# Kernel tuning notes

Measured on AMD Instinct MI355X. Metric: run time of the kernel, lower is better.

## Reference

```python
import jax, jax.numpy as jnp
import numpy as np

B, V, FIN, COUT, K = 16, 20000, 64, 64, 16


def setup_inputs() -> dict:
    key = jax.random.key(0)
    k1, k2, k3, k4 = jax.random.split(key, 4)
    x = jax.random.normal(k1, (B, V, FIN), dtype=jnp.float32)
    Wx = jax.random.normal(k2, (FIN, COUT), dtype=jnp.float32) * (1.0 / np.sqrt(FIN))
    Wn = jax.random.normal(k3, (FIN, COUT), dtype=jnp.float32) * (1.0 / np.sqrt(FIN))
    b = jnp.zeros((COUT,), dtype=jnp.float32)
    # neighbor indices into the padded input: 0 is the zero-padding row, 1..V are real vertices
    neighbor = jax.random.randint(k4, (V, K), 0, V + 1, dtype=jnp.int32)
    return {"x": x, "Wx": Wx, "Wn": Wn, "b": b, "neighbor": neighbor}


def reference(x, Wx, Wn, b, neighbor):
    # x: [B, V, Fin]; neighbor: [V, K] indices into padded (V+1) vertex axis
    Bsz, Vn, Fin = x.shape
    pad = jnp.zeros((Bsz, 1, Fin), dtype=x.dtype)
    padded = jnp.concatenate([pad, x], axis=1)            # [B, V+1, Fin]
    nb = padded[:, neighbor, :]                            # [B, V, K, Fin] (gather)
    nb_mean = jnp.mean(nb, axis=2)                         # sum/K == mean (zeros included)
    out = jnp.einsum('bvf,fc->bvc', x, Wx) \
        + jnp.einsum('bvf,fc->bvc', nb_mean, Wn) + b
    return out
```

## Files before the change

kernel.cpp:

```cpp
#include <hip/hip_runtime.h>
#include <hip/hip_bf16.h>

#define BATCH 16
#define NV    20000
#define FIN   64
#define NCOUT 64
#define NK    16
#define TOTROWS  (BATCH * NV)
#define NTILES   (TOTROWS / 16)

typedef __attribute__((ext_vector_type(8))) short bf16x8;
typedef __attribute__((ext_vector_type(4))) float f32x4;
typedef __attribute__((ext_vector_type(4))) unsigned short u16x4;

__device__ __forceinline__ short f2b(float f) {
    __hip_bfloat16 h = __float2bfloat16(f);
    return __builtin_bit_cast(short, h);
}

__global__ __launch_bounds__(256, 3) void convnet_gemm(
    const float* __restrict__ x,
    const float* __restrict__ Wx,
    const float* __restrict__ Wn,
    const float* __restrict__ bias,
    __hip_bfloat16* __restrict__ z,
    float* __restrict__ out)
{
    const int lane = threadIdx.x & 63;
    const int m    = lane & 15;
    const int quad = lane >> 4;

    bf16x8 bf[8][2];
#pragma unroll
    for (int t = 0; t < 8; ++t) {
        const float* W = (t < 4) ? Wx : Wn;
        const float scale = (t < 4) ? 1.0f : (1.0f / 16.0f);
        const int c = 4 * m + (t & 3);
#pragma unroll
        for (int h = 0; h < 2; ++h) {
            bf16x8 fr;
#pragma unroll
            for (int j = 0; j < 8; ++j) {
                const int f = 32 * h + quad * 8 + j;
                fr[j] = f2b(W[f * NCOUT + c] * scale);
            }
            bf[t][h] = fr;
        }
    }
    float bias_q[4];
#pragma unroll
    for (int t = 0; t < 4; ++t) bias_q[t] = bias[4 * m + t];

    const int nwaves = (gridDim.x * blockDim.x) >> 6;
    const int gw = (blockIdx.x * blockDim.x + threadIdx.x) >> 6;

    int rt = __builtin_amdgcn_readfirstlane(gw);
    const float* xt0 = x + (size_t)rt * (16 * FIN) + (size_t)m * FIN + quad * 8;
    float4 La0 = ((const float4*)xt0)[0];
    float4 La1 = ((const float4*)xt0)[1];
    float4 Lb0 = ((const float4*)(xt0 + 32))[0];
    float4 Lb1 = ((const float4*)(xt0 + 32))[1];

    for (;;) {
        bf16x8 af0, af1;
        af0[0] = f2b(La0.x); af0[1] = f2b(La0.y); af0[2] = f2b(La0.z); af0[3] = f2b(La0.w);
        af0[4] = f2b(La1.x); af0[5] = f2b(La1.y); af0[6] = f2b(La1.z); af0[7] = f2b(La1.w);
        af1[0] = f2b(Lb0.x); af1[1] = f2b(Lb0.y); af1[2] = f2b(Lb0.z); af1[3] = f2b(Lb0.w);
        af1[4] = f2b(Lb1.x); af1[5] = f2b(Lb1.y); af1[6] = f2b(Lb1.z); af1[7] = f2b(Lb1.w);

        const int rtn = rt + nwaves;
        const bool more = rtn < NTILES;
        float4 Na0, Na1, Nb0, Nb1;
        if (more) {
            const float* xn = x + (size_t)rtn * (16 * FIN) + (size_t)m * FIN + quad * 8;
            Na0 = ((const float4*)xn)[0];
            Na1 = ((const float4*)xn)[1];
            Nb0 = ((const float4*)(xn + 32))[0];
            Nb1 = ((const float4*)(xn + 32))[1];
        }

        f32x4 acc[8];
#pragma unroll
        for (int t = 0; t < 8; ++t) acc[t] = (f32x4){0.f, 0.f, 0.f, 0.f};
#pragma unroll
        for (int t = 0; t < 8; ++t)
            acc[t] = __builtin_amdgcn_mfma_f32_16x16x32_bf16(af0, bf[t][0], acc[t], 0, 0, 0);
#pragma unroll
        for (int t = 0; t < 8; ++t)
            acc[t] = __builtin_amdgcn_mfma_f32_16x16x32_bf16(af1, bf[t][1], acc[t], 0, 0, 0);

        const size_t rbase = (size_t)rt * 16 + quad * 4;
#pragma unroll
        for (int r = 0; r < 4; ++r) {
            const size_t orow = (rbase + r) * NCOUT + 4 * m;
            float4 o;
            o.x = acc[0][r] + bias_q[0];
            o.y = acc[1][r] + bias_q[1];
            o.z = acc[2][r] + bias_q[2];
            o.w = acc[3][r] + bias_q[3];
            *(float4*)(out + orow) = o;
            u16x4 zz;
            zz.x = (unsigned short)f2b(acc[4][r]);
            zz.y = (unsigned short)f2b(acc[5][r]);
            zz.z = (unsigned short)f2b(acc[6][r]);
            zz.w = (unsigned short)f2b(acc[7][r]);
            *(u16x4*)(z + orow) = zz;
        }

        if (!more) break;
        rt = __builtin_amdgcn_readfirstlane(rtn);
        La0 = Na0; La1 = Na1; Lb0 = Nb0; Lb1 = Nb1;
    }
}

__global__ __launch_bounds__(256, 6) void convnet_gather(
    const int* __restrict__ nbr,
    const __hip_bfloat16* __restrict__ z,
    float* __restrict__ out)
{
    const int lane = threadIdx.x & 63;
    const int s    = lane >> 4;
    const int c    = lane & 15;
    const int xcd  = blockIdx.x & 7;
    const int bi   = blockIdx.x >> 3;
    const int wl   = bi * (256 >> 6) + (threadIdx.x >> 6);
    const int WPX  = (gridDim.x >> 3) * (256 >> 6);

    const int nvoff = s * (NK * 4);
    const int zcol  = c * 8;
    const int GROUPS = (2 * NV) / 4;

    for (int g = wl; g < GROUPS; g += WPX) {
        const int gu = __builtin_amdgcn_readfirstlane(g);
        const int bl = (gu >= NV / 4) ? 1 : 0;
        const int b  = 2 * xcd + bl;
        const int v0 = gu * 4 - bl * NV;
        const int row0 = b * NV + v0;

        const int* nb = (const int*)((const char*)nbr + (size_t)v0 * (NK * 4) + nvoff);
        int id[NK];
#pragma unroll
        for (int k = 0; k < NK; ++k) id[k] = nb[k];

        const char* zb = (const char*)z + (size_t)b * NV * 128;
        float a0 = 0.f, a1 = 0.f, a2 = 0.f, a3 = 0.f;
#pragma unroll
        for (int k = 0; k < NK; ++k) {
            const int idx = id[k];
            int sel = idx - 1;
            sel = sel < 0 ? 0 : sel;
            const uint2 d = *(const uint2*)(zb + (size_t)(unsigned)(sel * 128 + zcol));
            const unsigned dx = idx ? d.x : 0u;
            const unsigned dy = idx ? d.y : 0u;
            a0 += __builtin_bit_cast(float, dx << 16);
            a1 += __builtin_bit_cast(float, dx & 0xFFFF0000u);
            a2 += __builtin_bit_cast(float, dy << 16);
            a3 += __builtin_bit_cast(float, dy & 0xFFFF0000u);
        }

        float4* o = (float4*)(out + (size_t)(row0 + s) * NCOUT + 4 * c);
        float4 ov = *o;
        ov.x += a0; ov.y += a1; ov.z += a2; ov.w += a3;
        *o = ov;
    }
}

extern "C" void kernel_launch(void* const* d_in, const int* in_sizes, int n_in,
                              void* d_out, int out_size, void* d_ws, size_t ws_size,
                              hipStream_t stream) {
    const float* x    = (const float*)d_in[0];
    const float* Wx   = (const float*)d_in[1];
    const float* Wn   = (const float*)d_in[2];
    const float* bias = (const float*)d_in[3];
    const int*   nbr  = (const int*)d_in[4];
    float* out = (float*)d_out;

    __hip_bfloat16* z = (__hip_bfloat16*)d_ws;

    hipLaunchKernelGGL(convnet_gemm, dim3(768), dim3(256), 0, stream,
                       x, Wx, Wn, bias, z, out);
    hipLaunchKernelGGL(convnet_gather, dim3(1536), dim3(256), 0, stream,
                       nbr, z, out);
}
```

Baseline: 225.1 us.

## Split GEMM accumulators, drop prefetch, XCD-map tiles, vectorize neighbor index loads

The GEMM kernel now maps tiles to XCDs in contiguous chunks and removes the software prefetch of the next tile. It computes the output half and the z half in two separate 4-accumulator phases to lower register pressure, with occupancy and grid raised to match. The gather kernel loads each row's 16 neighbor indices as four int4 loads instead of per-lane scalar loads, and issues the output read before the gather loop. Grid sizes and launch bounds are increased. Dropping the prefetch may expose global load latency, which the higher occupancy is meant to hide.

```diff
diff --git a/kernel.cpp b/kernel.cpp
--- a/kernel.cpp
+++ b/kernel.cpp
@@ -8,6 +8,7 @@
 #define NK    16
 #define TOTROWS  (BATCH * NV)
 #define NTILES   (TOTROWS / 16)
+#define TPX      (NTILES / 8)
 
 typedef __attribute__((ext_vector_type(8))) short bf16x8;
 typedef __attribute__((ext_vector_type(4))) float f32x4;
@@ -18,7 +19,7 @@
     return __builtin_bit_cast(short, h);
 }
 
-__global__ __launch_bounds__(256, 3) void convnet_gemm(
+__global__ __launch_bounds__(256, 4) void convnet_gemm(
     const float* __restrict__ x,
     const float* __restrict__ Wx,
     const float* __restrict__ Wn,
@@ -51,69 +52,75 @@
 #pragma unroll
     for (int t = 0; t < 4; ++t) bias_q[t] = bias[4 * m + t];
 
-    const int nwaves = (gridDim.x * blockDim.x) >> 6;
-    const int gw = (blockIdx.x * blockDim.x + threadIdx.x) >> 6;
+    const int xcd = blockIdx.x & 7;
+    const int bi  = blockIdx.x >> 3;
+    const int wl  = bi * 4 + ((int)threadIdx.x >> 6);
+    const int WPX = (gridDim.x >> 3) * 4;
 
-    int rt = __builtin_amdgcn_readfirstlane(gw);
-    const float* xt0 = x + (size_t)rt * (16 * FIN) + (size_t)m * FIN + quad * 8;
-    float4 La0 = ((const float4*)xt0)[0];
-    float4 La1 = ((const float4*)xt0)[1];
-    float4 Lb0 = ((const float4*)(xt0 + 32))[0];
-    float4 Lb1 = ((const float4*)(xt0 + 32))[1];
+    for (int t0 = wl; t0 < TPX; t0 += WPX) {
+        const int rt = __builtin_amdgcn_readfirstlane(xcd * TPX + t0);
+        const float* xt =
+            x + (size_t)rt * (16 * FIN) + (size_t)m * FIN + quad * 8;
 
-    for (;;) {
+        const float4 La0 = ((const float4*)xt)[0];
+        const float4 La1 = ((const float4*)xt)[1];
+        const float4 Lb0 = ((const float4*)(xt + 32))[0];
+        const float4 Lb1 = ((const float4*)(xt + 32))[1];
+
         bf16x8 af0, af1;
         af0[0] = f2b(La0.x); af0[1] = f2b(La0.y); af0[2] = f2b(La0.z); af0[3] = f2b(La0.w);
         af0[4] = f2b(La1.x); af0[5] = f2b(La1.y); af0[6] = f2b(La1.z); af0[7] = f2b(La1.w);
         af1[0] = f2b(Lb0.x); af1[1] = f2b(Lb0.y); af1[2] = f2b(Lb0.z); af1[3] = f2b(Lb0.w);
         af1[4] = f2b(Lb1.x); af1[5] = f2b(Lb1.y); af1[6] = f2b(Lb1.z); af1[7] = f2b(Lb1.w);
 
-        const int rtn = rt + nwaves;
-        const bool more = rtn < NTILES;
-        float4 Na0, Na1, Nb0, Nb1;
-        if (more) {
-            const float* xn = x + (size_t)rtn * (16 * FIN) + (size_t)m * FIN + quad * 8;
-            Na0 = ((const float4*)xn)[0];
-            Na1 = ((const float4*)xn)[1];
-            Nb0 = ((const float4*)(xn + 32))[0];
-            Nb1 = ((const float4*)(xn + 32))[1];
+        const size_t rbase = (size_t)rt * 16 + quad * 4;
+
+        {
+            f32x4 accP[4];
+#pragma unroll
+            for (int t = 0; t < 4; ++t) accP[t] = (f32x4){0.f, 0.f, 0.f, 0.f};
+#pragma unroll
+            for (int t = 0; t < 4; ++t)
+                accP[t] = __builtin_amdgcn_mfma_f32_16x16x32_bf16(af0, bf[t][0], accP[t], 0, 0, 0);
+#pragma unroll
+            for (int t = 0; t < 4; ++t)
+                accP[t] = __builtin_amdgcn_mfma_f32_16x16x32_bf16(af1, bf[t][1], accP[t], 0, 0, 0);
+#pragma unroll
+            for (int r = 0; r < 4; ++r) {
+                const size_t orow = (rbase + r) * NCOUT + 4 * m;
+                float4 o;
+                o.x = accP[0][r] + bias_q[0];
+                o.y = accP[1][r] + bias_q[1];
+                o.z = accP[2][r] + bias_q[2];
+                o.w = accP[3][r] + bias_q[3];
+                *(float4*)(out + orow) = o;
+            }
         }
-
-        f32x4 acc[8];
+        {
+            f32x4 accZ[4];
 #pragma unroll
-        for (int t = 0; t < 8; ++t) acc[t] = (f32x4){0.f, 0.f, 0.f, 0.f};
+            for (int t = 0; t < 4; ++t) accZ[t] = (f32x4){0.f, 0.f, 0.f, 0.f};
 #pragma unroll
-        for (int t = 0; t < 8; ++t)
-            acc[t] = __builtin_amdgcn_mfma_f32_16x16x32_bf16(af0, bf[t][0], acc[t], 0, 0, 0);
+            for (int t = 0; t < 4; ++t)
+                accZ[t] = __builtin_amdgcn_mfma_f32_16x16x32_bf16(af0, bf[t + 4][0], accZ[t], 0, 0, 0);
 #pragma unroll
-        for (int t = 0; t < 8; ++t)
-            acc[t] = __builtin_amdgcn_mfma_f32_16x16x32_bf16(af1, bf[t][1], acc[t], 0, 0, 0);
-
-        const size_t rbase = (size_t)rt * 16 + quad * 4;
+            for (int t = 0; t < 4; ++t)
+                accZ[t] = __builtin_amdgcn_mfma_f32_16x16x32_bf16(af1, bf[t + 4][1], accZ[t], 0, 0, 0);
 #pragma unroll
-        for (int r = 0; r < 4; ++r) {
-            const size_t orow = (rbase + r) * NCOUT + 4 * m;
-            float4 o;
-            o.x = acc[0][r] + bias_q[0];
-            o.y = acc[1][r] + bias_q[1];
-            o.z = acc[2][r] + bias_q[2];
-            o.w = acc[3][r] + bias_q[3];
-            *(float4*)(out + orow) = o;
-            u16x4 zz;
-            zz.x = (unsigned short)f2b(acc[4][r]);
-            zz.y = (unsigned short)f2b(acc[5][r]);
-            zz.z = (unsigned short)f2b(acc[6][r]);
-            zz.w = (unsigned short)f2b(acc[7][r]);
-            *(u16x4*)(z + orow) = zz;
+            for (int r = 0; r < 4; ++r) {
+                const size_t orow = (rbase + r) * NCOUT + 4 * m;
+                u16x4 zz;
+                zz.x = (unsigned short)f2b(accZ[0][r]);
+                zz.y = (unsigned short)f2b(accZ[1][r]);
+                zz.z = (unsigned short)f2b(accZ[2][r]);
+                zz.w = (unsigned short)f2b(accZ[3][r]);
+                *(u16x4*)(z + orow) = zz;
+            }
         }
-
-        if (!more) break;
-        rt = __builtin_amdgcn_readfirstlane(rtn);
-        La0 = Na0; La1 = Na1; Lb0 = Nb0; Lb1 = Nb1;
     }
 }
 
-__global__ __launch_bounds__(256, 6) void convnet_gather(
+__global__ __launch_bounds__(256, 8) void convnet_gather(
     const int* __restrict__ nbr,
     const __hip_bfloat16* __restrict__ z,
     float* __restrict__ out)
@@ -123,11 +130,10 @@
     const int c    = lane & 15;
     const int xcd  = blockIdx.x & 7;
     const int bi   = blockIdx.x >> 3;
-    const int wl   = bi * (256 >> 6) + (threadIdx.x >> 6);
-    const int WPX  = (gridDim.x >> 3) * (256 >> 6);
+    const int wl   = bi * 4 + ((int)threadIdx.x >> 6);
+    const int WPX  = (gridDim.x >> 3) * 4;
 
-    const int nvoff = s * (NK * 4);
-    const int zcol  = c * 8;
+    const int zcol   = c * 8;
     const int GROUPS = (2 * NV) / 4;
 
     for (int g = wl; g < GROUPS; g += WPX) {
@@ -137,10 +143,20 @@
         const int v0 = gu * 4 - bl * NV;
         const int row0 = b * NV + v0;
 
-        const int* nb = (const int*)((const char*)nbr + (size_t)v0 * (NK * 4) + nvoff);
+        float4* o = (float4*)(out + (size_t)(row0 + s) * NCOUT + 4 * c);
+        float4 ov = *o;
+
+        const int4* nb4 =
+            (const int4*)((const char*)nbr + (size_t)(v0 + s) * (NK * 4));
+        const int4 i0 = nb4[0];
+        const int4 i1 = nb4[1];
+        const int4 i2 = nb4[2];
+        const int4 i3 = nb4[3];
         int id[NK];
-#pragma unroll
-        for (int k = 0; k < NK; ++k) id[k] = nb[k];
+        id[0] = i0.x; id[1] = i0.y; id[2]  = i0.z; id[3]  = i0.w;
+        id[4] = i1.x; id[5] = i1.y; id[6]  = i1.z; id[7]  = i1.w;
+        id[8] = i2.x; id[9] = i2.y; id[10] = i2.z; id[11] = i2.w;
+        id[12] = i3.x; id[13] = i3.y; id[14] = i3.z; id[15] = i3.w;
 
         const char* zb = (const char*)z + (size_t)b * NV * 128;
         float a0 = 0.f, a1 = 0.f, a2 = 0.f, a3 = 0.f;
@@ -158,8 +174,6 @@
             a3 += __builtin_bit_cast(float, dy & 0xFFFF0000u);
         }
 
-        float4* o = (float4*)(out + (size_t)(row0 + s) * NCOUT + 4 * c);
-        float4 ov = *o;
         ov.x += a0; ov.y += a1; ov.z += a2; ov.w += a3;
         *o = ov;
     }
@@ -177,8 +191,8 @@
 
     __hip_bfloat16* z = (__hip_bfloat16*)d_ws;
 
-    hipLaunchKernelGGL(convnet_gemm, dim3(768), dim3(256), 0, stream,
+    hipLaunchKernelGGL(convnet_gemm, dim3(1024), dim3(256), 0, stream,
                        x, Wx, Wn, bias, z, out);
-    hipLaunchKernelGGL(convnet_gather, dim3(1536), dim3(256), 0, stream,
+    hipLaunchKernelGGL(convnet_gather, dim3(2048), dim3(256), 0, stream,
                        nbr, z, out);
 }
```

Result: slower. 232.1 us (+3.1%).
